# Kernel optimization log

Hardware: AMD Instinct MI355X
Metric: run time of the kernel (lower is better)

The kernel has to match this reference:

```python
import jax, jax.numpy as jnp
import numpy as np

B, S, D = 4, 2048, 768
H = 12
DH = D // H
FF = 4 * D
EPS = 1e-5


def _layernorm(x, g, b):
    mu = jnp.mean(x, axis=-1, keepdims=True)
    var = jnp.mean(jnp.square(x - mu), axis=-1, keepdims=True)
    return (x - mu) * jax.lax.rsqrt(var + EPS) * g + b


def setup_inputs() -> dict:
    key = jax.random.key(0)
    ks = jax.random.split(key, 16)
    s_d = 1.0 / np.sqrt(D)
    s_ff = 1.0 / np.sqrt(FF)
    inp = {
        "x": jax.random.normal(ks[0], (B, S, D), jnp.float32),
        # LayerNorm 1
        "ln1_g": jnp.ones((D,), jnp.float32),
        "ln1_b": jnp.zeros((D,), jnp.float32),
        # attention linears (stored as [in, out], i.e. already transposed)
        "Wq": jax.random.normal(ks[1], (D, D), jnp.float32) * s_d,
        "bq": jax.random.normal(ks[2], (D,), jnp.float32) * s_d,
        "Wk": jax.random.normal(ks[3], (D, D), jnp.float32) * s_d,
        "bk": jax.random.normal(ks[4], (D,), jnp.float32) * s_d,
        "Wv": jax.random.normal(ks[5], (D, D), jnp.float32) * s_d,
        "bv": jax.random.normal(ks[6], (D,), jnp.float32) * s_d,
        "Wo": jax.random.normal(ks[7], (D, D), jnp.float32) * s_d,
        "bo": jax.random.normal(ks[8], (D,), jnp.float32) * s_d,
        # LayerNorm 2
        "ln2_g": jnp.ones((D,), jnp.float32),
        "ln2_b": jnp.zeros((D,), jnp.float32),
        # feed-forward (bias always on, per torch code)
        "W1": jax.random.normal(ks[9], (D, FF), jnp.float32) * s_d,
        "b1": jax.random.normal(ks[10], (FF,), jnp.float32) * s_d,
        "W2": jax.random.normal(ks[11], (FF, D), jnp.float32) * s_ff,
        "b2": jax.random.normal(ks[12], (D,), jnp.float32) * s_ff,
    }
    return inp


def reference(x, ln1_g, ln1_b, Wq, bq, Wk, bk, Wv, bv, Wo, bo,
              ln2_g, ln2_b, W1, b1, W2, b2):
    # --- attention branch (pre-LN) ---
    h = _layernorm(x, ln1_g, ln1_b)
    q = (h @ Wq + bq).reshape(B, S, H, DH).transpose(0, 2, 1, 3)  # [B,H,S,DH]
    k = (h @ Wk + bk).reshape(B, S, H, DH).transpose(0, 2, 1, 3)
    v = (h @ Wv + bv).reshape(B, S, H, DH).transpose(0, 2, 1, 3)
    scores = jnp.einsum("bhqd,bhkd->bhqk", q, k) / np.sqrt(DH)
    causal = jnp.tril(jnp.ones((S, S), bool))
    scores = jnp.where(causal, scores, -jnp.inf)
    attn = jax.nn.softmax(scores, axis=-1)
    out = jnp.einsum("bhqk,bhkd->bhqd", attn, v)
    out = out.transpose(0, 2, 1, 3).reshape(B, S, D)
    x = x + (out @ Wo + bo)
    # --- feed-forward branch (pre-LN, exact GELU) ---
    h2 = _layernorm(x, ln2_g, ln2_b)
    ff = jax.nn.gelu(h2 @ W1 + b1, approximate=False) @ W2 + b2
    return x + ff
```

## Files before the change

kernel.cpp:

```cpp
#include <hip/hip_runtime.h>
#include <math.h>

#define B_ 4
#define S_ 2048
#define D_ 768
#define H_ 12
#define DH_ 64
#define FF_ 3072
#define LDQ (3*D_)

using short8  = __attribute__((ext_vector_type(8))) short;
using f32x4   = __attribute__((ext_vector_type(4))) float;
using f32x16  = __attribute__((ext_vector_type(16))) float;
using float4v = __attribute__((ext_vector_type(4))) float;
using ushort4v= __attribute__((ext_vector_type(4))) unsigned short;

__device__ __forceinline__ unsigned short f2bf(float f) {
  unsigned u = __builtin_bit_cast(unsigned, f);
  u += 0x7FFFu + ((u >> 16) & 1u);
  return (unsigned short)(u >> 16);
}

__device__ __forceinline__ unsigned cvt_pk_bf16(float a, float b) {
  unsigned r;
  asm("v_cvt_pk_bf16_f32 %0, %1, %2" : "=v"(r) : "v"(a), "v"(b));
  return r;
}

__device__ __forceinline__ float gelu_tanh(float x) {
  float x2 = x * x;
  float y  = x * fmaf(0.0356774081f, x2, 0.7978845608f);
  float e  = exp2f(y * 2.885390082f);
  float t  = 1.0f - 2.0f / (e + 1.0f);
  float hx = 0.5f * x;
  return fmaf(hx, t, hx);
}

__device__ __forceinline__ void gload16(const void* g, void* l) {
  __builtin_amdgcn_global_load_lds(
      (const __attribute__((address_space(1))) unsigned*)g,
      (__attribute__((address_space(3))) unsigned*)l, 16, 0, 0);
}

__global__ __launch_bounds__(256) void transpose_cast_multi_kernel(
    const float* __restrict__ Wq, const float* __restrict__ Wk,
    const float* __restrict__ Wv, const float* __restrict__ Wo,
    const float* __restrict__ W1, const float* __restrict__ W2,
    unsigned short* __restrict__ WqT, unsigned short* __restrict__ WkT,
    unsigned short* __restrict__ WvT, unsigned short* __restrict__ WoT,
    unsigned short* __restrict__ W1T, unsigned short* __restrict__ W2T) {
  __shared__ float tile[32][33];
  int bid = blockIdx.x;
  const float* in; unsigned short* out; int K, N, t;
  if (bid < 2304) {
    int seg = bid / 576; t = bid % 576; K = D_; N = D_;
    in  = seg == 0 ? Wq  : seg == 1 ? Wk  : seg == 2 ? Wv  : Wo;
    out = seg == 0 ? WqT : seg == 1 ? WkT : seg == 2 ? WvT : WoT;
  } else if (bid < 4608) {
    t = bid - 2304; K = D_; N = FF_; in = W1; out = W1T;
  } else {
    t = bid - 4608; K = FF_; N = D_; in = W2; out = W2T;
  }
  int ntk = K / 32;
  int k0 = (t % ntk) * 32, n0 = (t / ntk) * 32;
  int tx = threadIdx.x, ty = threadIdx.y;
#pragma unroll
  for (int i = 0; i < 4; i++)
    tile[ty + 8*i][tx] = in[(size_t)(k0 + ty + 8*i) * N + n0 + tx];
  __syncthreads();
#pragma unroll
  for (int i = 0; i < 4; i++)
    out[(size_t)(n0 + ty + 8*i) * K + k0 + tx] = f2bf(tile[tx][ty + 8*i]);
}

__global__ void bias_cat_kernel(const float* __restrict__ bq, const float* __restrict__ bk,
                                const float* __restrict__ bv, float* __restrict__ dst) {
  int i = blockIdx.x * 256 + threadIdx.x;
  if (i >= 3 * D_) return;
  float v;
  if (i < D_)            v = bq[i];
  else if (i < 2 * D_)   v = bk[i - D_];
  else                   v = bv[i - 2 * D_];
  dst[i] = v;
}

__global__ __launch_bounds__(256) void layernorm_kernel(
    const float* __restrict__ x, const float* __restrict__ g,
    const float* __restrict__ b, unsigned short* __restrict__ out) {
  int wave = threadIdx.x >> 6, lane = threadIdx.x & 63;
  int row = blockIdx.x * 4 + wave;
  const float* xr = x + (size_t)row * D_;
  float4v v[3];
  float sum = 0.f, sq = 0.f;
#pragma unroll
  for (int i = 0; i < 3; i++) {
    v[i] = reinterpret_cast<const float4v*>(xr)[lane + 64*i];
#pragma unroll
    for (int j = 0; j < 4; j++) { sum += v[i][j]; sq += v[i][j]*v[i][j]; }
  }
#pragma unroll
  for (int d = 1; d < 64; d <<= 1) { sum += __shfl_xor(sum, d); sq += __shfl_xor(sq, d); }
  float mu   = sum * (1.0f / D_);
  float var  = sq  * (1.0f / D_) - mu * mu;
  float rstd = rsqrtf(var + 1e-5f);
  unsigned short* orow = out + (size_t)row * D_;
#pragma unroll
  for (int i = 0; i < 3; i++) {
    int idx = (lane + 64*i) * 4;
    ushort4v o;
#pragma unroll
    for (int j = 0; j < 4; j++)
      o[j] = f2bf((v[i][j] - mu) * rstd * g[idx + j] + b[idx + j]);
    *reinterpret_cast<ushort4v*>(orow + idx) = o;
  }
}

#define EPI_QKV   0
#define EPI_OPROJ 1
#define EPI_GELU  2
#define EPI_FINAL 3

template<int EPI>
__global__ __launch_bounds__(256) void gemm_kernel(
    const unsigned short* __restrict__ A, int lda,
    const unsigned short* __restrict__ BT, int K,
    const float* __restrict__ bias,
    const float* __restrict__ resid,
    float* __restrict__ outf,
    unsigned short* __restrict__ outh,
    int ldo, float ascale, int nN) {
  __shared__ __attribute__((aligned(16))) unsigned short Ls[3][128*64];
  int tid = threadIdx.x;
  int wave = tid >> 6, lane = tid & 63;
  int lrow = lane & 15, lk = lane >> 4;
  int bid = blockIdx.x;
  int xcd = bid & 7, j = bid >> 3;
  int nM8 = gridDim.x / (8 * nN);
  int m0 = (xcd * nM8 + (j % nM8)) * 128;
  int n0 = (j / nM8) * 128;
  int wm = (wave >> 1) * 64, wn = (wave & 1) * 64;

  auto STAGE = [&](int buf, int k0) {
#pragma unroll
    for (int i = 0; i < 4; i++) {
      int ch = i * 256 + tid;
      int row = ch >> 3, s8 = ch & 7;
      int m = s8 ^ (row & 7);
      const unsigned short* src = (m < 4)
        ? A  + (size_t)(m0 + row) * lda + k0 + m * 8
        : BT + (size_t)(n0 + row) * K   + k0 + (m - 4) * 8;
      gload16(src, &Ls[buf][(i*256 + wave*64) * 8]);
    }
  };

  f32x4 acc[4][4] = {};
  int nt = K / 32;
  STAGE(0, 0);
  STAGE(1, 32);
  for (int t = 0; t < nt; t++) {
    if (t + 1 < nt) { asm volatile("s_waitcnt vmcnt(4)" ::: "memory"); }
    else            { asm volatile("s_waitcnt vmcnt(0)" ::: "memory"); }
    __builtin_amdgcn_s_barrier();
    const unsigned short* Lc = Ls[t % 3];
    short8 af[4], bf[4];
#pragma unroll
    for (int mi = 0; mi < 4; mi++) {
      int row = wm + mi*16 + lrow;
      af[mi] = *reinterpret_cast<const short8*>(&Lc[row*64 + ((lk ^ (row & 7)) * 8)]);
    }
#pragma unroll
    for (int ni = 0; ni < 4; ni++) {
      int row = wn + ni*16 + lrow;
      bf[ni] = *reinterpret_cast<const short8*>(&Lc[row*64 + (((4 + lk) ^ (row & 7)) * 8)]);
    }
    if (t + 2 < nt) STAGE((t + 2) % 3, (t + 2) * 32);
    __builtin_amdgcn_s_setprio(1);
#pragma unroll
    for (int mi = 0; mi < 4; mi++)
#pragma unroll
      for (int ni = 0; ni < 4; ni++)
        acc[mi][ni] = __builtin_amdgcn_mfma_f32_16x16x32_bf16(af[mi], bf[ni], acc[mi][ni], 0, 0, 0);
    __builtin_amdgcn_s_setprio(0);
  }
#pragma unroll
  for (int mi = 0; mi < 4; mi++) {
#pragma unroll
    for (int ni = 0; ni < 4; ni++) {
#pragma unroll
      for (int r = 0; r < 4; r++) {
        int gm = m0 + wm + mi*16 + (lane >> 4)*4 + r;
        int gn = n0 + wn + ni*16 + lrow;
        float v = acc[mi][ni][r] + bias[gn];
        if constexpr (EPI == EPI_QKV) {
          if (gn < D_) v *= ascale;
          float nb = __shfl_xor(v, 1);
          if (!(lane & 1))
            *reinterpret_cast<unsigned*>(&outh[(size_t)gm * ldo + gn]) = cvt_pk_bf16(v, nb);
        } else if constexpr (EPI == EPI_OPROJ) {
          size_t idx = (size_t)gm * ldo + gn;
          outf[idx] = v + resid[idx];
        } else if constexpr (EPI == EPI_GELU) {
          float gv = gelu_tanh(v);
          float nb = __shfl_xor(gv, 1);
          if (!(lane & 1))
            *reinterpret_cast<unsigned*>(&outh[(size_t)gm * ldo + gn]) = cvt_pk_bf16(gv, nb);
        } else {
          size_t idx = (size_t)gm * ldo + gn;
          outf[idx] = v + resid[idx];
        }
      }
    }
  }
}

__global__ __launch_bounds__(256, 3) void attn_kernel(
    const unsigned short* __restrict__ qkv,
    unsigned short* __restrict__ o) {
  __shared__ __attribute__((aligned(16))) unsigned short Ks[2][64*64];
  __shared__ __attribute__((aligned(16))) unsigned short VT[2][64*64];
  int tid = threadIdx.x;
  int wave = tid >> 6, lane = tid & 63;
  int ql = lane & 31, hi = lane >> 5;
  int bid = blockIdx.x;
  int xcd = bid & 7, r = bid >> 3;
  int bh = xcd * 6 + (r % 6);
  int qtile = 15 - (r / 6);
  int bb = bh / H_, hh = bh % H_;
  const unsigned short* qb = qkv + (size_t)bb * S_ * LDQ + hh * DH_;
  const unsigned short* kb = qb + D_;
  const unsigned short* vb = qb + 2 * D_;

  int sr = tid >> 2;
  int sc16 = (tid & 3) * 16;
  int kp = tid & 31, dh0 = (tid >> 5) * 8;
  uint4 krA, krB, vrA, vrB;

  auto LOADR = [&](int kb0) {
    const unsigned short* ksrc = kb + (size_t)(kb0 + sr) * LDQ + sc16;
    krA = *reinterpret_cast<const uint4*>(ksrc);
    krB = *reinterpret_cast<const uint4*>(ksrc + 8);
    const unsigned short* vsrc = vb + (size_t)(kb0 + 2*kp) * LDQ + dh0;
    vrA = *reinterpret_cast<const uint4*>(vsrc);
    vrB = *reinterpret_cast<const uint4*>(vsrc + LDQ);
  };
  auto WRITE = [&](int buf) {
    int sw = (sr & 7) << 4;
    int cb = sc16 * 2;
    *reinterpret_cast<uint4*>(&Ks[buf][(sr*128 + (cb ^ sw)) >> 1]) = krA;
    *reinterpret_cast<uint4*>(&Ks[buf][(sr*128 + ((cb + 16) ^ sw)) >> 1]) = krB;
    union { uint4 u4; unsigned short s[8]; } a, b;
    a.u4 = vrA; b.u4 = vrB;
#pragma unroll
    for (int j2 = 0; j2 < 8; j2++) {
      int row = dh0 + j2, sw2 = (row & 7) << 4;
      *reinterpret_cast<unsigned*>(&VT[buf][(row*128 + ((4*kp) ^ sw2)) >> 1]) =
          (unsigned)a.s[j2] | ((unsigned)b.s[j2] << 16);
    }
  };

  int q0 = qtile * 128;
  int qw = q0 + wave * 32;
  int myq = qw + ql;

  short8 qf[4];
#pragma unroll
  for (int dblk = 0; dblk < 4; dblk++)
    qf[dblk] = *reinterpret_cast<const short8*>(qb + (size_t)myq * LDQ + dblk*16 + hi*8);

  f32x16 oaccT[2] = {};
  float mst = -1e30f, lst = 0.f;
  int nt = q0 / 64 + 2;

  auto TILE = [&](int kt, int cur) {
    int kb0 = kt * 64;
    bool has_next = (kt + 1 < nt);
    if (has_next) LOADR((kt + 1) * 64);

    if (kb0 <= qw + 31) {
      f32x16 sc[2] = {};
      __builtin_amdgcn_s_setprio(1);
#pragma unroll
      for (int dblk = 0; dblk < 4; dblk++) {
#pragma unroll
        for (int blk = 0; blk < 2; blk++) {
          int row = blk*32 + ql;
          int sw = (row & 7) << 4;
          short8 kf = *reinterpret_cast<const short8*>(
              &Ks[cur][(row*128 + (((unsigned)(dblk*32 + hi*16)) ^ sw)) >> 1]);
          sc[blk] = __builtin_amdgcn_mfma_f32_32x32x16_bf16(kf, qf[dblk], sc[blk], 0, 0, 0);
        }
      }
      __builtin_amdgcn_s_setprio(0);
      bool full = (kb0 + 63 <= qw);
      if (!full) {
#pragma unroll
        for (int blk = 0; blk < 2; blk++)
#pragma unroll
          for (int r2 = 0; r2 < 16; r2++) {
            int key = kb0 + blk*32 + (r2 & 3) + 8*(r2 >> 2) + 4*hi;
            if (key > myq) sc[blk][r2] = -1e30f;
          }
      }
      float pm0 = -1e30f, pm1 = -1e30f, pm2 = -1e30f, pm3 = -1e30f;
#pragma unroll
      for (int blk = 0; blk < 2; blk++)
#pragma unroll
        for (int g = 0; g < 4; g++) {
          pm0 = fmaxf(pm0, sc[blk][4*g]);
          pm1 = fmaxf(pm1, sc[blk][4*g+1]);
          pm2 = fmaxf(pm2, sc[blk][4*g+2]);
          pm3 = fmaxf(pm3, sc[blk][4*g+3]);
        }
      float mx = fmaxf(fmaxf(pm0, pm1), fmaxf(pm2, pm3));
      mx = fmaxf(mx, __shfl_xor(mx, 32));
      if (!__all(mx <= mst + 8.0f)) {
        float mnew = fmaxf(mst, mx);
        float fac = exp2f(mst - mnew);
        lst *= fac;
#pragma unroll
        for (int db = 0; db < 2; db++)
#pragma unroll
          for (int r2 = 0; r2 < 16; r2++) oaccT[db][r2] *= fac;
        mst = mnew;
      }
      short8 pa[4];
      float rs = 0.f;
#pragma unroll
      for (int b = 0; b < 2; b++) {
#pragma unroll
        for (int so = 0; so < 2; so++) {
          float p0 = exp2f(sc[b][8*so + 0] - mst);
          float p1 = exp2f(sc[b][8*so + 1] - mst);
          float p2 = exp2f(sc[b][8*so + 2] - mst);
          float p3 = exp2f(sc[b][8*so + 3] - mst);
          float p4 = exp2f(sc[b][8*so + 4] - mst);
          float p5 = exp2f(sc[b][8*so + 5] - mst);
          float p6 = exp2f(sc[b][8*so + 6] - mst);
          float p7 = exp2f(sc[b][8*so + 7] - mst);
          rs += ((p0 + p1) + (p2 + p3)) + ((p4 + p5) + (p6 + p7));
          unsigned W0 = cvt_pk_bf16(p0, p1);
          unsigned W1 = cvt_pk_bf16(p2, p3);
          unsigned W2 = cvt_pk_bf16(p4, p5);
          unsigned W3 = cvt_pk_bf16(p6, p7);
          asm volatile("v_permlane32_swap_b32 %0, %1" : "+v"(W0), "+v"(W2));
          asm volatile("v_permlane32_swap_b32 %0, %1" : "+v"(W1), "+v"(W3));
          union { uint4 u; short8 s; } cvtu;
          cvtu.u.x = W0; cvtu.u.y = W1; cvtu.u.z = W2; cvtu.u.w = W3;
          pa[2*b + so] = cvtu.s;
        }
      }
      rs += __shfl_xor(rs, 32);
      lst += rs;
      __builtin_amdgcn_s_setprio(1);
#pragma unroll
      for (int ks = 0; ks < 4; ks++) {
        int cb = ks*32 + hi*16;
#pragma unroll
        for (int db = 0; db < 2; db++) {
          int row = db*32 + ql;
          int sw = (row & 7) << 4;
          short8 vf = *reinterpret_cast<const short8*>(&VT[cur][(row*128 + (cb ^ sw)) >> 1]);
          oaccT[db] = __builtin_amdgcn_mfma_f32_32x32x16_bf16(vf, pa[ks], oaccT[db], 0, 0, 0);
        }
      }
      __builtin_amdgcn_s_setprio(0);
    }

    if (has_next) WRITE(cur ^ 1);
    __syncthreads();
  };

  LOADR(0);
  WRITE(0);
  __syncthreads();
  for (int kt = 0; kt < nt; kt += 2) {
    TILE(kt, 0);
    TILE(kt + 1, 1);
  }

  float inv = 1.0f / lst;
  unsigned short* ob = o + ((size_t)(bb * S_ + myq)) * D_ + hh * DH_;
#pragma unroll
  for (int db = 0; db < 2; db++)
#pragma unroll
    for (int g = 0; g < 8; g++) {
      int r2 = 2 * g;
      int dh = db*32 + (r2 & 3) + 8*(r2 >> 2) + 4*hi;
      unsigned pk = cvt_pk_bf16(oaccT[db][r2] * inv, oaccT[db][r2+1] * inv);
      *reinterpret_cast<unsigned*>(ob + dh) = pk;
    }
}

extern "C" void kernel_launch(void* const* d_in, const int* in_sizes, int n_in,
                              void* d_out, int out_size, void* d_ws, size_t ws_size,
                              hipStream_t stream) {
  (void)in_sizes; (void)n_in; (void)out_size; (void)ws_size;
  const float* x    = (const float*)d_in[0];
  const float* ln1g = (const float*)d_in[1];
  const float* ln1b = (const float*)d_in[2];
  const float* Wq   = (const float*)d_in[3];
  const float* bq   = (const float*)d_in[4];
  const float* Wk   = (const float*)d_in[5];
  const float* bk   = (const float*)d_in[6];
  const float* Wv   = (const float*)d_in[7];
  const float* bv   = (const float*)d_in[8];
  const float* Wo   = (const float*)d_in[9];
  const float* bo   = (const float*)d_in[10];
  const float* ln2g = (const float*)d_in[11];
  const float* ln2b = (const float*)d_in[12];
  const float* W1   = (const float*)d_in[13];
  const float* b1   = (const float*)d_in[14];
  const float* W2   = (const float*)d_in[15];
  const float* b2   = (const float*)d_in[16];
  float* out = (float*)d_out;

  char* ws = (char*)d_ws;
  size_t off = 0;
  auto alloc = [&](size_t bytes) {
    char* p = ws + off;
    off += (bytes + 255) & ~(size_t)255;
    return p;
  };
  unsigned short* WqT = (unsigned short*)alloc((size_t)D_*D_*2);
  unsigned short* WkT = (unsigned short*)alloc((size_t)D_*D_*2);
  unsigned short* WvT = (unsigned short*)alloc((size_t)D_*D_*2);
  unsigned short* WoT = (unsigned short*)alloc((size_t)D_*D_*2);
  unsigned short* W1T = (unsigned short*)alloc((size_t)D_*FF_*2);
  unsigned short* W2T = (unsigned short*)alloc((size_t)FF_*D_*2);
  unsigned short* h   = (unsigned short*)alloc((size_t)B_*S_*D_*2);
  unsigned short* qkv = (unsigned short*)alloc((size_t)B_*S_*LDQ*2);
  unsigned short* ob  = (unsigned short*)alloc((size_t)B_*S_*D_*2);
  float* bias_cat     = (float*)alloc((size_t)3*D_*4);
  unsigned short* ffb = qkv;
  unsigned short* h2  = h;

  const float qscale = 0.125f * 1.4426950408889634f;

  dim3 tb(32, 8);
  transpose_cast_multi_kernel<<<6912, tb, 0, stream>>>(
      Wq, Wk, Wv, Wo, W1, W2, WqT, WkT, WvT, WoT, W1T, W2T);
  bias_cat_kernel<<<9, 256, 0, stream>>>(bq, bk, bv, bias_cat);

  layernorm_kernel<<<(B_*S_)/4, 256, 0, stream>>>(x, ln1g, ln1b, h);

  gemm_kernel<EPI_QKV><<<dim3(64*18), 256, 0, stream>>>(
      h, D_, WqT, D_, bias_cat, nullptr, nullptr, qkv, LDQ, qscale, 18);

  attn_kernel<<<dim3(768), 256, 0, stream>>>(qkv, ob);

  gemm_kernel<EPI_OPROJ><<<dim3(64*6), 256, 0, stream>>>(
      ob, D_, WoT, D_, bo, x, out, nullptr, D_, 1.0f, 6);

  layernorm_kernel<<<(B_*S_)/4, 256, 0, stream>>>(out, ln2g, ln2b, h2);

  gemm_kernel<EPI_GELU><<<dim3(64*24), 256, 0, stream>>>(
      h2, D_, W1T, D_, b1, nullptr, nullptr, ffb, FF_, 1.0f, 24);

  gemm_kernel<EPI_FINAL><<<dim3(64*6), 256, 0, stream>>>(
      ffb, FF_, W2T, FF_, b2, out, out, nullptr, D_, 1.0f, 6);
}
```

Measured before the change: 262.3 us.

## Widen GEMM block tile to 128x256 with split A/B LDS and precomputed offsets

The GEMM block tile grows from 128x128 to 128x256. Each wave now computes a 64x128 sub-tile with 4x8 MFMA accumulators, so every loaded A fragment is reused twice as often. Shared memory is split into separate A and B triple buffers using a row-paired swizzled layout, and the global source pointers and LDS read offsets are computed once before the K loop. Grid sizes are halved to match. This cuts global and LDS traffic per FLOP, but doubles register pressure and leaves only 192 blocks for the N=768 GEMMs, which may underfill the GPU.

```diff
diff --git a/kernel.cpp b/kernel.cpp
--- a/kernel.cpp
+++ b/kernel.cpp
@@ -121,7 +121,7 @@
 #define EPI_FINAL 3
 
 template<int EPI>
-__global__ __launch_bounds__(256) void gemm_kernel(
+__global__ __launch_bounds__(256, 2) void gemm_kernel(
     const unsigned short* __restrict__ A, int lda,
     const unsigned short* __restrict__ BT, int K,
     const float* __restrict__ bias,
@@ -129,63 +129,83 @@
     float* __restrict__ outf,
     unsigned short* __restrict__ outh,
     int ldo, float ascale, int nN) {
-  __shared__ __attribute__((aligned(16))) unsigned short Ls[3][128*64];
+  __shared__ __attribute__((aligned(16))) unsigned short As[3][64*64];
+  __shared__ __attribute__((aligned(16))) unsigned short Bs[3][128*64];
   int tid = threadIdx.x;
   int wave = tid >> 6, lane = tid & 63;
   int lrow = lane & 15, lk = lane >> 4;
   int bid = blockIdx.x;
   int xcd = bid & 7, j = bid >> 3;
-  int nM8 = gridDim.x / (8 * nN);
-  int m0 = (xcd * nM8 + (j % nM8)) * 128;
-  int n0 = (j / nM8) * 128;
-  int wm = (wave >> 1) * 64, wn = (wave & 1) * 64;
-
+  int m0 = (xcd * 8 + (j & 7)) * 128;
+  int n0 = (j >> 3) * 256;
+  int wm = (wave & 1) * 64, wn = (wave >> 1) * 128;
+
+  const unsigned short* srcA[2];
+  const unsigned short* srcB[4];
+#pragma unroll
+  for (int i = 0; i < 2; i++) {
+    int ch = i * 256 + tid;
+    int ur = ch >> 3, m = (ch & 7) ^ (ur & 7);
+    srcA[i] = A + (size_t)(m0 + 2*ur + (m >> 2)) * lda + (m & 3) * 8;
+  }
+#pragma unroll
+  for (int i = 0; i < 4; i++) {
+    int ch = i * 256 + tid;
+    int ur = ch >> 3, m = (ch & 7) ^ (ur & 7);
+    srcB[i] = BT + (size_t)(n0 + 2*ur + (m >> 2)) * K + (m & 3) * 8;
+  }
   auto STAGE = [&](int buf, int k0) {
 #pragma unroll
-    for (int i = 0; i < 4; i++) {
-      int ch = i * 256 + tid;
-      int row = ch >> 3, s8 = ch & 7;
-      int m = s8 ^ (row & 7);
-      const unsigned short* src = (m < 4)
-        ? A  + (size_t)(m0 + row) * lda + k0 + m * 8
-        : BT + (size_t)(n0 + row) * K   + k0 + (m - 4) * 8;
-      gload16(src, &Ls[buf][(i*256 + wave*64) * 8]);
-    }
+    for (int i = 0; i < 2; i++)
+      gload16(srcA[i] + k0, &As[buf][(i*256 + wave*64) * 8]);
+#pragma unroll
+    for (int i = 0; i < 4; i++)
+      gload16(srcB[i] + k0, &Bs[buf][(i*256 + wave*64) * 8]);
   };
 
-  f32x4 acc[4][4] = {};
+  int offA[4], offB[8];
+#pragma unroll
+  for (int mi = 0; mi < 4; mi++) {
+    int row = wm + mi*16 + lrow, ur = row >> 1;
+    offA[mi] = ur*64 + (((((row & 1) << 2) | lk) ^ (ur & 7)) * 8);
+  }
+#pragma unroll
+  for (int ni = 0; ni < 8; ni++) {
+    int row = wn + ni*16 + lrow, ur = row >> 1;
+    offB[ni] = ur*64 + (((((row & 1) << 2) | lk) ^ (ur & 7)) * 8);
+  }
+
+  f32x4 acc[4][8] = {};
   int nt = K / 32;
   STAGE(0, 0);
   STAGE(1, 32);
   for (int t = 0; t < nt; t++) {
-    if (t + 1 < nt) { asm volatile("s_waitcnt vmcnt(4)" ::: "memory"); }
+    if (t + 1 < nt) { asm volatile("s_waitcnt vmcnt(6)" ::: "memory"); }
     else            { asm volatile("s_waitcnt vmcnt(0)" ::: "memory"); }
     __builtin_amdgcn_s_barrier();
-    const unsigned short* Lc = Ls[t % 3];
-    short8 af[4], bf[4];
-#pragma unroll
-    for (int mi = 0; mi < 4; mi++) {
-      int row = wm + mi*16 + lrow;
-      af[mi] = *reinterpret_cast<const short8*>(&Lc[row*64 + ((lk ^ (row & 7)) * 8)]);
-    }
-#pragma unroll
-    for (int ni = 0; ni < 4; ni++) {
-      int row = wn + ni*16 + lrow;
-      bf[ni] = *reinterpret_cast<const short8*>(&Lc[row*64 + (((4 + lk) ^ (row & 7)) * 8)]);
-    }
+    int slot = t % 3;
+    const unsigned short* Ac = As[slot];
+    const unsigned short* Bc = Bs[slot];
+    short8 af[4], bf[8];
+#pragma unroll
+    for (int mi = 0; mi < 4; mi++)
+      af[mi] = *reinterpret_cast<const short8*>(&Ac[offA[mi]]);
+#pragma unroll
+    for (int ni = 0; ni < 8; ni++)
+      bf[ni] = *reinterpret_cast<const short8*>(&Bc[offB[ni]]);
     if (t + 2 < nt) STAGE((t + 2) % 3, (t + 2) * 32);
     __builtin_amdgcn_s_setprio(1);
 #pragma unroll
     for (int mi = 0; mi < 4; mi++)
 #pragma unroll
-      for (int ni = 0; ni < 4; ni++)
+      for (int ni = 0; ni < 8; ni++)
         acc[mi][ni] = __builtin_amdgcn_mfma_f32_16x16x32_bf16(af[mi], bf[ni], acc[mi][ni], 0, 0, 0);
     __builtin_amdgcn_s_setprio(0);
   }
 #pragma unroll
   for (int mi = 0; mi < 4; mi++) {
 #pragma unroll
-    for (int ni = 0; ni < 4; ni++) {
+    for (int ni = 0; ni < 8; ni++) {
 #pragma unroll
       for (int r = 0; r < 4; r++) {
         int gm = m0 + wm + mi*16 + (lane >> 4)*4 + r;
@@ -443,19 +463,19 @@
 
   layernorm_kernel<<<(B_*S_)/4, 256, 0, stream>>>(x, ln1g, ln1b, h);
 
-  gemm_kernel<EPI_QKV><<<dim3(64*18), 256, 0, stream>>>(
-      h, D_, WqT, D_, bias_cat, nullptr, nullptr, qkv, LDQ, qscale, 18);
+  gemm_kernel<EPI_QKV><<<dim3(8*8*9), 256, 0, stream>>>(
+      h, D_, WqT, D_, bias_cat, nullptr, nullptr, qkv, LDQ, qscale, 9);
 
   attn_kernel<<<dim3(768), 256, 0, stream>>>(qkv, ob);
 
-  gemm_kernel<EPI_OPROJ><<<dim3(64*6), 256, 0, stream>>>(
-      ob, D_, WoT, D_, bo, x, out, nullptr, D_, 1.0f, 6);
+  gemm_kernel<EPI_OPROJ><<<dim3(8*8*3), 256, 0, stream>>>(
+      ob, D_, WoT, D_, bo, x, out, nullptr, D_, 1.0f, 3);
 
   layernorm_kernel<<<(B_*S_)/4, 256, 0, stream>>>(out, ln2g, ln2b, h2);
 
-  gemm_kernel<EPI_GELU><<<dim3(64*24), 256, 0, stream>>>(
-      h2, D_, W1T, D_, b1, nullptr, nullptr, ffb, FF_, 1.0f, 24);
-
-  gemm_kernel<EPI_FINAL><<<dim3(64*6), 256, 0, stream>>>(
-      ffb, FF_, W2T, FF_, b2, out, out, nullptr, D_, 1.0f, 6);
-}
+  gemm_kernel<EPI_GELU><<<dim3(8*8*12), 256, 0, stream>>>(
+      h2, D_, W1T, D_, b1, nullptr, nullptr, ffb, FF_, 1.0f, 12);
+
+  gemm_kernel<EPI_FINAL><<<dim3(8*8*3), 256, 0, stream>>>(
+      ffb, FF_, W2T, FF_, b2, out, out, nullptr, D_, 1.0f, 3);
+}
```

Result: slower. 301.0 us (+14.8%).

## Add 256x256-tile GEMM kernel with split-phase pipelining for QKV and FFN1

Applied to the files above, without the earlier changes.

Introduces a new 512-thread GEMM that computes 256x256 output tiles, using a three-slot LDS ring with swizzled layout. Each K-step is split into two halves, and the A and B prefetch loads are interleaved between the MFMA halves under raised wave priority. The QKV and W1 projections now use it instead of the 128-row kernel, which raises arithmetic intensity and reduces global/LDS traffic per FLOP. The trade-off is fewer blocks (288 and 384), which risks wave-quantization imbalance on the GPU's CUs, plus heavier register pressure from 32 accumulator tiles per wave.

```diff
diff --git a/kernel.cpp b/kernel.cpp
--- a/kernel.cpp
+++ b/kernel.cpp
@@ -119,6 +119,117 @@
 #define EPI_OPROJ 1
 #define EPI_GELU  2
 #define EPI_FINAL 3
+
+template<int EPI>
+__global__ __launch_bounds__(512, 2) void gemm256_kernel(
+    const unsigned short* __restrict__ A, int lda,
+    const unsigned short* __restrict__ BT, int K,
+    const float* __restrict__ bias,
+    unsigned short* __restrict__ outh,
+    int ldo, float ascale) {
+  __shared__ __attribute__((aligned(16))) unsigned short As[3][256*32];
+  __shared__ __attribute__((aligned(16))) unsigned short Bs[3][256*32];
+  int tid = threadIdx.x;
+  int wid = tid >> 6, lane = tid & 63;
+  int lrow = lane & 15, lk = lane >> 4;
+  int bid = blockIdx.x;
+  int xcd = bid & 7, j = bid >> 3;
+  int m0 = (xcd * 4 + (j & 3)) * 256;
+  int n0 = (j >> 2) * 256;
+  int wm = (wid >> 2) * 128, wn = (wid & 3) * 64;
+
+  const unsigned short* srcA[2];
+  const unsigned short* srcB[2];
+#pragma unroll
+  for (int i = 0; i < 2; i++) {
+    int ch = i * 512 + tid;
+    int ur = ch >> 3, m = (ch & 7) ^ (ur & 7);
+    srcA[i] = A  + (size_t)(m0 + 2*ur + (m >> 2)) * lda + (m & 3) * 8;
+    srcB[i] = BT + (size_t)(n0 + 2*ur + (m >> 2)) * K   + (m & 3) * 8;
+  }
+  auto STAGE_A = [&](int buf, int k0) {
+#pragma unroll
+    for (int i = 0; i < 2; i++)
+      gload16(srcA[i] + k0, &As[buf][(i*512 + wid*64) * 8]);
+  };
+  auto STAGE_B = [&](int buf, int k0) {
+#pragma unroll
+    for (int i = 0; i < 2; i++)
+      gload16(srcB[i] + k0, &Bs[buf][(i*512 + wid*64) * 8]);
+  };
+
+  int offA[8], offB[4];
+#pragma unroll
+  for (int mi = 0; mi < 8; mi++) {
+    int row = wm + mi*16 + lrow, ur = row >> 1;
+    offA[mi] = ur*64 + (((((row & 1) << 2) | lk) ^ (ur & 7)) * 8);
+  }
+#pragma unroll
+  for (int ni = 0; ni < 4; ni++) {
+    int row = wn + ni*16 + lrow, ur = row >> 1;
+    offB[ni] = ur*64 + (((((row & 1) << 2) | lk) ^ (ur & 7)) * 8);
+  }
+
+  f32x4 acc[8][4] = {};
+  int nc = K / 32;
+  STAGE_A(0, 0); STAGE_B(0, 0);
+  STAGE_A(1, 32); STAGE_B(1, 32);
+  for (int t = 0; t < nc; t++) {
+    if (t + 1 < nc) { asm volatile("s_waitcnt vmcnt(4)" ::: "memory"); }
+    else            { asm volatile("s_waitcnt vmcnt(0)" ::: "memory"); }
+    __builtin_amdgcn_s_barrier();
+    int slot = t % 3;
+    const unsigned short* Ac = As[slot];
+    const unsigned short* Bc = Bs[slot];
+    short8 af[8], bf[4];
+#pragma unroll
+    for (int mi = 0; mi < 4; mi++)
+      af[mi] = *reinterpret_cast<const short8*>(&Ac[offA[mi]]);
+#pragma unroll
+    for (int ni = 0; ni < 4; ni++)
+      bf[ni] = *reinterpret_cast<const short8*>(&Bc[offB[ni]]);
+    if (t + 2 < nc) STAGE_A((t + 2) % 3, (t + 2) * 32);
+    __builtin_amdgcn_s_setprio(1);
+#pragma unroll
+    for (int mi = 0; mi < 4; mi++)
+#pragma unroll
+      for (int ni = 0; ni < 4; ni++)
+        acc[mi][ni] = __builtin_amdgcn_mfma_f32_16x16x32_bf16(af[mi], bf[ni], acc[mi][ni], 0, 0, 0);
+    __builtin_amdgcn_s_setprio(0);
+    __builtin_amdgcn_s_barrier();
+#pragma unroll
+    for (int mi = 4; mi < 8; mi++)
+      af[mi] = *reinterpret_cast<const short8*>(&Ac[offA[mi]]);
+    if (t + 2 < nc) STAGE_B((t + 2) % 3, (t + 2) * 32);
+    __builtin_amdgcn_s_setprio(1);
+#pragma unroll
+    for (int mi = 4; mi < 8; mi++)
+#pragma unroll
+      for (int ni = 0; ni < 4; ni++)
+        acc[mi][ni] = __builtin_amdgcn_mfma_f32_16x16x32_bf16(af[mi], bf[ni], acc[mi][ni], 0, 0, 0);
+    __builtin_amdgcn_s_setprio(0);
+  }
+#pragma unroll
+  for (int mi = 0; mi < 8; mi++) {
+#pragma unroll
+    for (int ni = 0; ni < 4; ni++) {
+#pragma unroll
+      for (int r = 0; r < 4; r++) {
+        int gm = m0 + wm + mi*16 + (lane >> 4)*4 + r;
+        int gn = n0 + wn + ni*16 + lrow;
+        float v = acc[mi][ni][r] + bias[gn];
+        if constexpr (EPI == EPI_QKV) {
+          if (gn < D_) v *= ascale;
+        } else {
+          v = gelu_tanh(v);
+        }
+        float nb = __shfl_xor(v, 1);
+        if (!(lane & 1))
+          *reinterpret_cast<unsigned*>(&outh[(size_t)gm * ldo + gn]) = cvt_pk_bf16(v, nb);
+      }
+    }
+  }
+}
 
 template<int EPI>
 __global__ __launch_bounds__(256) void gemm_kernel(
@@ -443,8 +554,8 @@
 
   layernorm_kernel<<<(B_*S_)/4, 256, 0, stream>>>(x, ln1g, ln1b, h);
 
-  gemm_kernel<EPI_QKV><<<dim3(64*18), 256, 0, stream>>>(
-      h, D_, WqT, D_, bias_cat, nullptr, nullptr, qkv, LDQ, qscale, 18);
+  gemm256_kernel<EPI_QKV><<<dim3(8*4*9), 512, 0, stream>>>(
+      h, D_, WqT, D_, bias_cat, qkv, LDQ, qscale);
 
   attn_kernel<<<dim3(768), 256, 0, stream>>>(qkv, ob);
 
@@ -453,8 +564,8 @@
 
   layernorm_kernel<<<(B_*S_)/4, 256, 0, stream>>>(out, ln2g, ln2b, h2);
 
-  gemm_kernel<EPI_GELU><<<dim3(64*24), 256, 0, stream>>>(
-      h2, D_, W1T, D_, b1, nullptr, nullptr, ffb, FF_, 1.0f, 24);
+  gemm256_kernel<EPI_GELU><<<dim3(8*4*12), 512, 0, stream>>>(
+      h2, D_, W1T, D_, b1, ffb, FF_, 1.0f);
 
   gemm_kernel<EPI_FINAL><<<dim3(64*6), 256, 0, stream>>>(
       ffb, FF_, W2T, FF_, b2, out, out, nullptr, D_, 1.0f, 6);
```

Result: slower. 292.6 us (+11.5%).

## Merge prep kernels into one launch and use 64-row tiles for N=768 GEMMs

Applied to the files above, without the earlier changes.

Folds the weight transpose/cast, the bias concatenation and the first layernorm into a single prep kernel, removing two launches. Adds a new GEMM kernel with 64x128 tiles and a 3-stage LDS pipeline for the O-projection and FF2 GEMMs (N=768). These previously launched only 384 blocks, and the new kernel launches 768 to fill more CUs. The smaller tiles add some redundant B-operand traffic, and the new residual epilogue writes unpacked fp32 scalars.

```diff
diff --git a/kernel.cpp b/kernel.cpp
--- a/kernel.cpp
+++ b/kernel.cpp
@@ -42,46 +42,78 @@
       (__attribute__((address_space(3))) unsigned*)l, 16, 0, 0);
 }
 
-__global__ __launch_bounds__(256) void transpose_cast_multi_kernel(
+__global__ __launch_bounds__(256) void prep_kernel(
     const float* __restrict__ Wq, const float* __restrict__ Wk,
     const float* __restrict__ Wv, const float* __restrict__ Wo,
     const float* __restrict__ W1, const float* __restrict__ W2,
     unsigned short* __restrict__ WqT, unsigned short* __restrict__ WkT,
     unsigned short* __restrict__ WvT, unsigned short* __restrict__ WoT,
-    unsigned short* __restrict__ W1T, unsigned short* __restrict__ W2T) {
+    unsigned short* __restrict__ W1T, unsigned short* __restrict__ W2T,
+    const float* __restrict__ bq, const float* __restrict__ bk,
+    const float* __restrict__ bv, float* __restrict__ bias_cat,
+    const float* __restrict__ x, const float* __restrict__ ln1g,
+    const float* __restrict__ ln1b, unsigned short* __restrict__ h) {
   __shared__ float tile[32][33];
   int bid = blockIdx.x;
-  const float* in; unsigned short* out; int K, N, t;
-  if (bid < 2304) {
-    int seg = bid / 576; t = bid % 576; K = D_; N = D_;
-    in  = seg == 0 ? Wq  : seg == 1 ? Wk  : seg == 2 ? Wv  : Wo;
-    out = seg == 0 ? WqT : seg == 1 ? WkT : seg == 2 ? WvT : WoT;
-  } else if (bid < 4608) {
-    t = bid - 2304; K = D_; N = FF_; in = W1; out = W1T;
+  int tid = threadIdx.x;
+  if (bid < 6912) {
+    const float* in; unsigned short* out; int K, N, t;
+    if (bid < 2304) {
+      int seg = bid / 576; t = bid % 576; K = D_; N = D_;
+      in  = seg == 0 ? Wq  : seg == 1 ? Wk  : seg == 2 ? Wv  : Wo;
+      out = seg == 0 ? WqT : seg == 1 ? WkT : seg == 2 ? WvT : WoT;
+    } else if (bid < 4608) {
+      t = bid - 2304; K = D_; N = FF_; in = W1; out = W1T;
+    } else {
+      t = bid - 4608; K = FF_; N = D_; in = W2; out = W2T;
+    }
+    int ntk = K / 32;
+    int k0 = (t % ntk) * 32, n0 = (t / ntk) * 32;
+    int tx = tid & 31, ty = tid >> 5;
+#pragma unroll
+    for (int i = 0; i < 4; i++)
+      tile[ty + 8*i][tx] = in[(size_t)(k0 + ty + 8*i) * N + n0 + tx];
+    __syncthreads();
+#pragma unroll
+    for (int i = 0; i < 4; i++)
+      out[(size_t)(n0 + ty + 8*i) * K + k0 + tx] = f2bf(tile[tx][ty + 8*i]);
+  } else if (bid < 6921) {
+    int i = (bid - 6912) * 256 + tid;
+    if (i < 3 * D_) {
+      float v;
+      if (i < D_)            v = bq[i];
+      else if (i < 2 * D_)   v = bk[i - D_];
+      else                   v = bv[i - 2 * D_];
+      bias_cat[i] = v;
+    }
   } else {
-    t = bid - 4608; K = FF_; N = D_; in = W2; out = W2T;
-  }
-  int ntk = K / 32;
-  int k0 = (t % ntk) * 32, n0 = (t / ntk) * 32;
-  int tx = threadIdx.x, ty = threadIdx.y;
-#pragma unroll
-  for (int i = 0; i < 4; i++)
-    tile[ty + 8*i][tx] = in[(size_t)(k0 + ty + 8*i) * N + n0 + tx];
-  __syncthreads();
-#pragma unroll
-  for (int i = 0; i < 4; i++)
-    out[(size_t)(n0 + ty + 8*i) * K + k0 + tx] = f2bf(tile[tx][ty + 8*i]);
-}
-
-__global__ void bias_cat_kernel(const float* __restrict__ bq, const float* __restrict__ bk,
-                                const float* __restrict__ bv, float* __restrict__ dst) {
-  int i = blockIdx.x * 256 + threadIdx.x;
-  if (i >= 3 * D_) return;
-  float v;
-  if (i < D_)            v = bq[i];
-  else if (i < 2 * D_)   v = bk[i - D_];
-  else                   v = bv[i - 2 * D_];
-  dst[i] = v;
+    int wave = tid >> 6, lane = tid & 63;
+    int row = (bid - 6921) * 4 + wave;
+    const float* xr = x + (size_t)row * D_;
+    float4v v[3];
+    float sum = 0.f, sq = 0.f;
+#pragma unroll
+    for (int i = 0; i < 3; i++) {
+      v[i] = reinterpret_cast<const float4v*>(xr)[lane + 64*i];
+#pragma unroll
+      for (int j = 0; j < 4; j++) { sum += v[i][j]; sq += v[i][j]*v[i][j]; }
+    }
+#pragma unroll
+    for (int d = 1; d < 64; d <<= 1) { sum += __shfl_xor(sum, d); sq += __shfl_xor(sq, d); }
+    float mu   = sum * (1.0f / D_);
+    float var  = sq  * (1.0f / D_) - mu * mu;
+    float rstd = rsqrtf(var + 1e-5f);
+    unsigned short* orow = h + (size_t)row * D_;
+#pragma unroll
+    for (int i = 0; i < 3; i++) {
+      int idx = (lane + 64*i) * 4;
+      ushort4v o;
+#pragma unroll
+      for (int j = 0; j < 4; j++)
+        o[j] = f2bf((v[i][j] - mu) * rstd * ln1g[idx + j] + ln1b[idx + j]);
+      *reinterpret_cast<ushort4v*>(orow + idx) = o;
+    }
+  }
 }
 
 __global__ __launch_bounds__(256) void layernorm_kernel(
@@ -208,6 +240,97 @@
           size_t idx = (size_t)gm * ldo + gn;
           outf[idx] = v + resid[idx];
         }
+      }
+    }
+  }
+}
+
+template<int EPI>
+__global__ __launch_bounds__(256) void gemm_n64_kernel(
+    const unsigned short* __restrict__ A, int lda,
+    const unsigned short* __restrict__ BT, int K,
+    const float* __restrict__ bias,
+    const float* __restrict__ resid,
+    float* __restrict__ outf, int ldo) {
+  __shared__ __attribute__((aligned(16))) unsigned short As[3][64*32];
+  __shared__ __attribute__((aligned(16))) unsigned short Bs[3][128*32];
+  int tid = threadIdx.x;
+  int wave = tid >> 6, lane = tid & 63;
+  int lrow = lane & 15, lk = lane >> 4;
+  int bid = blockIdx.x;
+  int xcd = bid & 7, j = bid >> 3;
+  int m0 = (xcd * 16 + (j % 16)) * 64;
+  int n0 = (j / 16) * 128;
+  int wm = (wave >> 1) * 32, wn = (wave & 1) * 64;
+
+  const unsigned short* srcA;
+  const unsigned short* srcB[2];
+  {
+    int r = tid >> 2, m = (tid & 3) ^ (r & 3);
+    srcA = A + (size_t)(m0 + r) * lda + m * 8;
+  }
+#pragma unroll
+  for (int i = 0; i < 2; i++) {
+    int ch = i * 256 + tid;
+    int r = ch >> 2, m = (ch & 3) ^ (r & 3);
+    srcB[i] = BT + (size_t)(n0 + r) * K + m * 8;
+  }
+  auto STAGE = [&](int buf, int k0) {
+    gload16(srcA + k0, &As[buf][(wave*64) * 8]);
+#pragma unroll
+    for (int i = 0; i < 2; i++)
+      gload16(srcB[i] + k0, &Bs[buf][(i*256 + wave*64) * 8]);
+  };
+
+  int offA[2], offB[4];
+#pragma unroll
+  for (int mi = 0; mi < 2; mi++) {
+    int row = wm + mi*16 + lrow;
+    offA[mi] = row*32 + ((lk ^ (row & 3)) * 8);
+  }
+#pragma unroll
+  for (int ni = 0; ni < 4; ni++) {
+    int row = wn + ni*16 + lrow;
+    offB[ni] = row*32 + ((lk ^ (row & 3)) * 8);
+  }
+
+  f32x4 acc[2][4] = {};
+  int nt = K / 32;
+  STAGE(0, 0);
+  STAGE(1, 32);
+  for (int t = 0; t < nt; t++) {
+    if (t + 1 < nt) { asm volatile("s_waitcnt vmcnt(3)" ::: "memory"); }
+    else            { asm volatile("s_waitcnt vmcnt(0)" ::: "memory"); }
+    __builtin_amdgcn_s_barrier();
+    int slot = t % 3;
+    const unsigned short* Ac = As[slot];
+    const unsigned short* Bc = Bs[slot];
+    short8 af[2], bf[4];
+#pragma unroll
+    for (int mi = 0; mi < 2; mi++)
+      af[mi] = *reinterpret_cast<const short8*>(&Ac[offA[mi]]);
+#pragma unroll
+    for (int ni = 0; ni < 4; ni++)
+      bf[ni] = *reinterpret_cast<const short8*>(&Bc[offB[ni]]);
+    if (t + 2 < nt) STAGE((t + 2) % 3, (t + 2) * 32);
+    __builtin_amdgcn_s_setprio(1);
+#pragma unroll
+    for (int mi = 0; mi < 2; mi++)
+#pragma unroll
+      for (int ni = 0; ni < 4; ni++)
+        acc[mi][ni] = __builtin_amdgcn_mfma_f32_16x16x32_bf16(af[mi], bf[ni], acc[mi][ni], 0, 0, 0);
+    __builtin_amdgcn_s_setprio(0);
+  }
+#pragma unroll
+  for (int mi = 0; mi < 2; mi++) {
+#pragma unroll
+    for (int ni = 0; ni < 4; ni++) {
+#pragma unroll
+      for (int r = 0; r < 4; r++) {
+        int gm = m0 + wm + mi*16 + (lane >> 4)*4 + r;
+        int gn = n0 + wn + ni*16 + lrow;
+        size_t idx = (size_t)gm * ldo + gn;
+        outf[idx] = acc[mi][ni][r] + bias[gn] + resid[idx];
       }
     }
   }
@@ -436,26 +559,23 @@
 
   const float qscale = 0.125f * 1.4426950408889634f;
 
-  dim3 tb(32, 8);
-  transpose_cast_multi_kernel<<<6912, tb, 0, stream>>>(
-      Wq, Wk, Wv, Wo, W1, W2, WqT, WkT, WvT, WoT, W1T, W2T);
-  bias_cat_kernel<<<9, 256, 0, stream>>>(bq, bk, bv, bias_cat);
-
-  layernorm_kernel<<<(B_*S_)/4, 256, 0, stream>>>(x, ln1g, ln1b, h);
+  prep_kernel<<<8969, 256, 0, stream>>>(
+      Wq, Wk, Wv, Wo, W1, W2, WqT, WkT, WvT, WoT, W1T, W2T,
+      bq, bk, bv, bias_cat, x, ln1g, ln1b, h);
 
   gemm_kernel<EPI_QKV><<<dim3(64*18), 256, 0, stream>>>(
       h, D_, WqT, D_, bias_cat, nullptr, nullptr, qkv, LDQ, qscale, 18);
 
   attn_kernel<<<dim3(768), 256, 0, stream>>>(qkv, ob);
 
-  gemm_kernel<EPI_OPROJ><<<dim3(64*6), 256, 0, stream>>>(
-      ob, D_, WoT, D_, bo, x, out, nullptr, D_, 1.0f, 6);
+  gemm_n64_kernel<EPI_OPROJ><<<dim3(768), 256, 0, stream>>>(
+      ob, D_, WoT, D_, bo, x, out, D_);
 
   layernorm_kernel<<<(B_*S_)/4, 256, 0, stream>>>(out, ln2g, ln2b, h2);
 
   gemm_kernel<EPI_GELU><<<dim3(64*24), 256, 0, stream>>>(
       h2, D_, W1T, D_, b1, nullptr, nullptr, ffb, FF_, 1.0f, 24);
 
-  gemm_kernel<EPI_FINAL><<<dim3(64*6), 256, 0, stream>>>(
-      ffb, FF_, W2T, FF_, b2, out, out, nullptr, D_, 1.0f, 6);
-}
+  gemm_n64_kernel<EPI_FINAL><<<dim3(768), 256, 0, stream>>>(
+      ffb, FF_, W2T, FF_, b2, out, out, D_);
+}
```

Result: no change. 267.0 us (+1.8%).
